# Kernel optimization log

Hardware: AMD Instinct MI355X
Metric: run time of the kernel (lower is better)

Reference implementation:

```python
import math
import jax, jax.numpy as jnp
import numpy as np

B, S, HID = 2, 2048, 1024
NH, HD = 16, 64            # num heads, head dim (HID = NH*HD)
NB, MAXD = 32, 128         # relative attention buckets / max distance
Q_SCALING = 1.0


def setup_inputs() -> dict:
    key = jax.random.key(0)
    ks = jax.random.split(key, 6)
    return {
        "hidden_states": jax.random.normal(ks[0], (B, S, HID), dtype=jnp.float32),
        "w_qkv": jax.random.normal(ks[1], (HID, 3 * HID), dtype=jnp.float32) * 0.02,
        "b_qkv": jax.random.normal(ks[2], (3 * HID,), dtype=jnp.float32) * 0.02,
        "w_dense": jax.random.normal(ks[3], (HID, HID), dtype=jnp.float32) * 0.02,
        "b_dense": jax.random.normal(ks[4], (HID,), dtype=jnp.float32) * 0.02,
        "rel_attn_table": jax.random.normal(ks[5], (NH, NB), dtype=jnp.float32) * 0.02,
    }


def _relative_position_bucket(q_len, k_len, num_buckets, max_distance):
    # Bidirectional T5-style buckets, matching compute_relative_bias.
    ctx = jnp.arange(q_len, dtype=jnp.int32)[:, None]
    mem = jnp.arange(k_len, dtype=jnp.int32)[None, :]
    rel = mem - ctx                                     # [Q, K]
    nb = num_buckets // 2
    buckets = jnp.where(rel > 0, nb, 0)
    rel = jnp.abs(rel)
    max_exact = nb // 2
    is_small = rel < max_exact
    # log path (clamp to >=1 to avoid log(0); masked by is_small anyway)
    tmp = jnp.log(jnp.maximum(rel, 1).astype(jnp.float32) / max_exact)
    large = tmp / math.log(max_distance / max_exact) * (nb - max_exact)
    large = max_exact + large.astype(jnp.int32)
    large = jnp.minimum(large, nb - 1)
    return buckets + jnp.where(is_small, rel, large)    # [Q, K]


def reference(hidden_states, w_qkv, b_qkv, w_dense, b_dense, rel_attn_table):
    b, s, _ = hidden_states.shape
    qkv = hidden_states @ w_qkv + b_qkv                 # [B, S, 3*HID]
    q, k, v = jnp.split(qkv, 3, axis=-1)
    q = q.reshape(b, s, NH, HD)
    k = k.reshape(b, s, NH, HD)
    v = v.reshape(b, s, NH, HD)

    norm = Q_SCALING * math.sqrt(HD)
    scores = jnp.einsum("bqhd,bkhd->bhqk", q, k) / norm  # [B, H, S, S]

    buckets = _relative_position_bucket(s, s, NB, MAXD)  # [Q, K] int32
    bias = rel_attn_table[:, buckets]                    # [H, Q, K]
    scores = scores + bias[None]

    probs = jax.nn.softmax(scores, axis=-1)
    ctx = jnp.einsum("bhqk,bkhd->bqhd", probs, v).reshape(b, s, HID)
    return ctx @ w_dense + b_dense
```

## Files before the change

### kernel.cpp

```cpp
#include <hip/hip_runtime.h>
#include <hip/hip_bf16.h>
#include <math.h>

#define S_ 2048

typedef __attribute__((ext_vector_type(8))) short bf16x8;
typedef __attribute__((ext_vector_type(4))) float f32x4;
typedef __attribute__((ext_vector_type(8))) unsigned short u16x8;
typedef __attribute__((ext_vector_type(4))) unsigned short u16x4;

__device__ inline unsigned short f2bf(float f) {
  union { float f; unsigned u; } x; x.f = f;
  unsigned r = x.u + 0x7fff + ((x.u >> 16) & 1);
  return (unsigned short)(r >> 16);
}

__device__ __forceinline__ float exp2_raw(float x) {
  float r;
  asm("v_exp_f32 %0, %1" : "=v"(r) : "v"(x));
  return r;
}

__device__ __forceinline__ void gll16(const unsigned short* g, unsigned short* l) {
  __builtin_amdgcn_global_load_lds(
      (const __attribute__((address_space(1))) unsigned int*)g,
      (__attribute__((address_space(3))) unsigned int*)l, 16, 0, 0);
}

__global__ void bias_table_kernel(const float* __restrict__ table,
                                  float* __restrict__ biasTab) {
  int idx = blockIdx.x * blockDim.x + threadIdx.x;
  if (idx >= 16 * 4096) return;
  int h = idx >> 12;
  int r = idx & 4095;
  int rel = r - 2047;
  int bucket = rel > 0 ? 16 : 0;
  int ar = rel < 0 ? -rel : rel;
  if (ar < 8) {
    bucket += ar;
  } else {
    float tmp = logf((float)ar / 8.0f);
    float lf = tmp / 2.7725887222397811f * 8.0f;
    int large = 8 + (int)lf;
    bucket += (large < 15 ? large : 15);
  }
  biasTab[idx] = table[h * 32 + bucket] * 1.44269504088896f;
}

__global__ __launch_bounds__(256) void cvt_bf16_kernel(
    const float* __restrict__ in, unsigned short* __restrict__ out, int n8) {
  int i = blockIdx.x * blockDim.x + threadIdx.x;
  if (i >= n8) return;
  float4 a = ((const float4*)in)[i * 2];
  float4 b = ((const float4*)in)[i * 2 + 1];
  u16x8 o;
  o[0] = f2bf(a.x); o[1] = f2bf(a.y); o[2] = f2bf(a.z); o[3] = f2bf(a.w);
  o[4] = f2bf(b.x); o[5] = f2bf(b.y); o[6] = f2bf(b.z); o[7] = f2bf(b.w);
  *(u16x8*)&out[(size_t)i * 8] = o;
}

__global__ __launch_bounds__(256) void transpose_cvt_kernel(
    const float* __restrict__ in, unsigned short* __restrict__ out,
    int K, int N) {
  __shared__ unsigned short tile[64][72];
  const int k0 = blockIdx.y * 64, n0 = blockIdx.x * 64;
  const int tid = threadIdx.x;
  const int rr = tid >> 4, cc = (tid & 15) * 4;
#pragma unroll
  for (int p = 0; p < 4; ++p) {
    int k = rr + p * 16;
    float4 v = *(const float4*)&in[(size_t)(k0 + k) * N + n0 + cc];
    tile[k][cc + 0] = f2bf(v.x);
    tile[k][cc + 1] = f2bf(v.y);
    tile[k][cc + 2] = f2bf(v.z);
    tile[k][cc + 3] = f2bf(v.w);
  }
  __syncthreads();
#pragma unroll
  for (int p = 0; p < 4; ++p) {
    int n = rr + p * 16;
    u16x4 o;
    o[0] = tile[cc + 0][n];
    o[1] = tile[cc + 1][n];
    o[2] = tile[cc + 2][n];
    o[3] = tile[cc + 3][n];
    *(u16x4*)&out[(size_t)(n0 + n) * K + k0 + cc] = o;
  }
}

template <bool BF16OUT>
__global__ __launch_bounds__(256) void gemm_mfma_kernel(
    const unsigned short* __restrict__ A, const unsigned short* __restrict__ Bt,
    const float* __restrict__ bias, void* __restrict__ Cout,
    int M, int N, int K) {
  __shared__ __align__(16) unsigned short As[128 * 32];
  __shared__ __align__(16) unsigned short Bs[128 * 32];
  const int tid = threadIdx.x;
  const int wave = tid >> 6, lane = tid & 63;
  const int lg = lane >> 4, lr = lane & 15;
  const int m0 = blockIdx.y * 128, n0 = blockIdx.x * 128;
  const int wm = (wave & 1) * 64, wn = (wave >> 1) * 64;

  f32x4 acc[4][4] = {};

  const int r0 = tid >> 2;
  const int sw = ((tid & 3) ^ (r0 & 3)) << 3;
  const unsigned short* aP0 = A + (size_t)(m0 + r0) * K + sw;
  const unsigned short* aP1 = A + (size_t)(m0 + 64 + r0) * K + sw;
  const unsigned short* bP0 = Bt + (size_t)(n0 + r0) * K + sw;
  const unsigned short* bP1 = Bt + (size_t)(n0 + 64 + r0) * K + sw;
  unsigned short* ldsA0 = &As[(tid & ~63) * 8];
  unsigned short* ldsA1 = &As[(256 + (tid & ~63)) * 8];
  unsigned short* ldsB0 = &Bs[(tid & ~63) * 8];
  unsigned short* ldsB1 = &Bs[(256 + (tid & ~63)) * 8];

  const int swz = (lg ^ (lr & 3)) << 3;

  for (int kt = 0; kt < K; kt += 32) {
    __syncthreads();
    gll16(aP0 + kt, ldsA0);
    gll16(aP1 + kt, ldsA1);
    gll16(bP0 + kt, ldsB0);
    gll16(bP1 + kt, ldsB1);
    __syncthreads();
    bf16x8 af[4], bfr[4];
#pragma unroll
    for (int t = 0; t < 4; ++t) {
      af[t]  = *(const bf16x8*)&As[(wm + t * 16 + lr) * 32 + swz];
      bfr[t] = *(const bf16x8*)&Bs[(wn + t * 16 + lr) * 32 + swz];
    }
#pragma unroll
    for (int i = 0; i < 4; ++i)
#pragma unroll
      for (int j = 0; j < 4; ++j)
        acc[i][j] = __builtin_amdgcn_mfma_f32_16x16x32_bf16(
            af[i], bfr[j], acc[i][j], 0, 0, 0);
  }

  float bv[4];
#pragma unroll
  for (int j = 0; j < 4; ++j) bv[j] = bias[n0 + wn + j * 16 + lr];
#pragma unroll
  for (int i = 0; i < 4; ++i) {
#pragma unroll
    for (int j = 0; j < 4; ++j) {
#pragma unroll
      for (int r = 0; r < 4; ++r) {
        int row = m0 + wm + i * 16 + lg * 4 + r;
        int col = n0 + wn + j * 16 + lr;
        float val = acc[i][j][r] + bv[j];
        if constexpr (BF16OUT)
          ((unsigned short*)Cout)[(size_t)row * N + col] = f2bf(val);
        else
          ((float*)Cout)[(size_t)row * N + col] = val;
      }
    }
  }
}

__global__ __launch_bounds__(256) void vperm_kernel(
    const unsigned short* __restrict__ qkvb, unsigned short* __restrict__ vP) {
  const int t = blockIdx.x, h = blockIdx.y, bb = blockIdx.z;
  __shared__ unsigned short tile[64][72];
  const int tid = threadIdx.x;
  {
    int k = tid >> 2, c = (tid & 3) * 16;
    const unsigned short* src =
        qkvb + (size_t)(bb * S_ + t * 64 + k) * 3072 + 2048 + h * 64 + c;
    *(bf16x8*)&tile[k][c] = *(const bf16x8*)src;
    *(bf16x8*)&tile[k][c + 8] = *(const bf16x8*)(src + 8);
  }
  __syncthreads();
  const int d = tid >> 2, m0 = (tid & 3) * 16;
  unsigned short* dst =
      vP + ((size_t)((bb * 16 + h) * 64 + d)) * S_ + t * 64 + m0;
#pragma unroll
  for (int half = 0; half < 2; ++half) {
    u16x8 o;
#pragma unroll
    for (int j = 0; j < 8; ++j) {
      int m = m0 + half * 8 + j;
      int phys_s = m >> 3, e = m & 7;
      int s = phys_s ^ (d & 7);
      int w = s >> 2, lg = s & 3;
      int kw = w * 32 + (e >> 2) * 16 + lg * 4 + (e & 3);
      o[j] = tile[kw][d];
    }
    *(u16x8*)(dst + half * 8) = o;
  }
}

__global__ __launch_bounds__(512) void attn_mfma6_kernel(
    const unsigned short* __restrict__ qkvb, const unsigned short* __restrict__ vP,
    const float* __restrict__ biasTab, unsigned short* __restrict__ ctxb) {
  const int wg0 = blockIdx.x;
  const int wg = (wg0 & 7) * 64 + (wg0 >> 3);
  const int qt = wg & 15;
  const int h  = (wg >> 4) & 15;
  const int bb = wg >> 8;

  const int tid = threadIdx.x;
  const int wave = tid >> 6;
  const int lane = tid & 63;
  const int lg = lane >> 4;
  const int lr = lane & 15;

  __shared__ __align__(16) unsigned short Klds[2][4096];
  __shared__ __align__(16) unsigned short Vlds[2][4096];
  __shared__ float biasW[2][192];

  const int q0 = qt * 128;
  const int qw = q0 + wave * 16;
  const float SCL = 0.125f * 1.44269504088896f;
  const float THR = 11.5415603f;

  bf16x8 qf[2];
#pragma unroll
  for (int kh = 0; kh < 2; ++kh)
    qf[kh] = *(const bf16x8*)(qkvb +
        (size_t)(bb * S_ + qw + lr) * 3072 + h * 64 + kh * 32 + lg * 8);

  float mrun = -1e30f;
  float lpart = 0.f;
  f32x4 ov[4] = {};

  const int kk = tid >> 3, kpb = tid & 7;
  const unsigned short* kptr = qkvb + (size_t)(bb * S_ + kk) * 3072 + 1024 +
                               h * 64 + (kpb ^ (kk & 7)) * 8;
  const unsigned short* vptr = vP + ((size_t)((bb * 16 + h) * 64 + (tid >> 3))) * S_ +
                               (tid & 7) * 8;
  const float* btabH = biasTab + h * 4096 + 2047;

  auto nonuni = [&](int tt) {
    int rl = tt * 64 - q0;
    return !((rl - 127 >= 91) || (rl + 63 <= -91));
  };

  gll16(kptr, &Klds[0][(tid & ~63) * 8]);
  gll16(vptr, &Vlds[0][(tid & ~63) * 8]);
  if (nonuni(0) && tid < 192) biasW[0][tid] = btabH[-q0 - 127 + tid];

  for (int t = 0; t < 32; ++t) {
    const int cur = t & 1;
    __syncthreads();

    if (t < 31) {
      const size_t kadv = (size_t)(t + 1) * 64 * 3072;
      gll16(kptr + kadv, &Klds[cur ^ 1][(tid & ~63) * 8]);
      gll16(vptr + (t + 1) * 64, &Vlds[cur ^ 1][(tid & ~63) * 8]);
      if (nonuni(t + 1) && tid < 192)
        biasW[cur ^ 1][tid] = btabH[(t + 1) * 64 - q0 - 127 + tid];
    }

    f32x4 sc[4] = {};
#pragma unroll
    for (int kt = 0; kt < 4; ++kt) {
      const unsigned short* kr = &Klds[cur][(kt * 16 + lr) * 64];
      bf16x8 kf0 = *(const bf16x8*)(kr + ((lg)     ^ (lr & 7)) * 8);
      bf16x8 kf1 = *(const bf16x8*)(kr + ((4 + lg) ^ (lr & 7)) * 8);
      sc[kt] = __builtin_amdgcn_mfma_f32_16x16x32_bf16(kf0, qf[0], sc[kt], 0, 0, 0);
      sc[kt] = __builtin_amdgcn_mfma_f32_16x16x32_bf16(kf1, qf[1], sc[kt], 0, 0, 0);
    }

    float pp[4][4];
    if (nonuni(t)) {
      const int bidx = 127 + lg * 4 - wave * 16 - lr;
#pragma unroll
      for (int kt = 0; kt < 4; ++kt)
#pragma unroll
        for (int r = 0; r < 4; ++r)
          pp[kt][r] = sc[kt][r] * SCL + biasW[cur][bidx + kt * 16 + r];
    } else {
      const float cb = btabH[t * 64 - q0];
#pragma unroll
      for (int kt = 0; kt < 4; ++kt)
#pragma unroll
        for (int r = 0; r < 4; ++r)
          pp[kt][r] = sc[kt][r] * SCL + cb;
    }

    float mx[8];
#pragma unroll
    for (int i = 0; i < 8; ++i)
      mx[i] = fmaxf(pp[i >> 1][(i & 1) * 2], pp[i >> 1][(i & 1) * 2 + 1]);
    float m01 = fmaxf(mx[0], mx[1]), m23 = fmaxf(mx[2], mx[3]);
    float m45 = fmaxf(mx[4], mx[5]), m67 = fmaxf(mx[6], mx[7]);
    float tm = fmaxf(fmaxf(m01, m23), fmaxf(m45, m67));

    if (!__all(tm <= mrun + THR)) {
      tm = fmaxf(tm, __shfl_xor(tm, 16));
      tm = fmaxf(tm, __shfl_xor(tm, 32));
      float mn = fmaxf(mrun, tm);
      float sfv = exp2_raw(mrun - mn);
      mrun = mn;
      lpart *= sfv;
#pragma unroll
      for (int r = 0; r < 4; ++r) {
        float sq = __shfl(sfv, (lane & 48) | (lg * 4 + r));
#pragma unroll
        for (int db = 0; db < 4; ++db) ov[db][r] *= sq;
      }
    }

#pragma unroll
    for (int kt = 0; kt < 4; ++kt)
#pragma unroll
      for (int r = 0; r < 4; ++r)
        pp[kt][r] = exp2_raw(pp[kt][r] - mrun);
    float s8[8];
#pragma unroll
    for (int i = 0; i < 8; ++i)
      s8[i] = pp[i >> 1][(i & 1) * 2] + pp[i >> 1][(i & 1) * 2 + 1];
    float s01 = s8[0] + s8[1], s23 = s8[2] + s8[3];
    float s45 = s8[4] + s8[5], s67 = s8[6] + s8[7];
    lpart += (s01 + s23) + (s45 + s67);

    union { bf16x8 v; unsigned u[4]; } pk[2];
#pragma unroll
    for (int kh = 0; kh < 2; ++kh) {
      asm("v_cvt_pk_bf16_f32 %0, %1, %2"
          : "=v"(pk[kh].u[0]) : "v"(pp[2 * kh][0]), "v"(pp[2 * kh][1]));
      asm("v_cvt_pk_bf16_f32 %0, %1, %2"
          : "=v"(pk[kh].u[1]) : "v"(pp[2 * kh][2]), "v"(pp[2 * kh][3]));
      asm("v_cvt_pk_bf16_f32 %0, %1, %2"
          : "=v"(pk[kh].u[2]) : "v"(pp[2 * kh + 1][0]), "v"(pp[2 * kh + 1][1]));
      asm("v_cvt_pk_bf16_f32 %0, %1, %2"
          : "=v"(pk[kh].u[3]) : "v"(pp[2 * kh + 1][2]), "v"(pp[2 * kh + 1][3]));
    }

#pragma unroll
    for (int kh = 0; kh < 2; ++kh)
#pragma unroll
      for (int db = 0; db < 4; ++db) {
        bf16x8 vf = *(const bf16x8*)&Vlds[cur][
            (db * 16 + lr) * 64 + ((4 * kh + lg) ^ (lr & 7)) * 8];
        ov[db] = __builtin_amdgcn_mfma_f32_16x16x32_bf16(
            pk[kh].v, vf, ov[db], 0, 0, 0);
      }
  }

  float lsum = lpart;
  lsum += __shfl_xor(lsum, 16);
  lsum += __shfl_xor(lsum, 32);
  float invl = 1.0f / lsum;
#pragma unroll
  for (int r = 0; r < 4; ++r) {
    float iv = __shfl(invl, (lane & 48) | (lg * 4 + r));
    size_t row = (size_t)(bb * S_ + qw + lg * 4 + r);
#pragma unroll
    for (int db = 0; db < 4; ++db)
      ctxb[row * 1024 + h * 64 + db * 16 + lr] = f2bf(ov[db][r] * iv);
  }
}

extern "C" void kernel_launch(void* const* d_in, const int* in_sizes, int n_in,
                              void* d_out, int out_size, void* d_ws, size_t ws_size,
                              hipStream_t stream) {
  const float* hs      = (const float*)d_in[0];
  const float* w_qkv   = (const float*)d_in[1];
  const float* b_qkv   = (const float*)d_in[2];
  const float* w_dense = (const float*)d_in[3];
  const float* b_dense = (const float*)d_in[4];
  const float* rtab    = (const float*)d_in[5];
  float* out = (float*)d_out;

  char* ws = (char*)d_ws;
  unsigned short* qkvb = (unsigned short*)ws;
  unsigned short* ctxb = (unsigned short*)(ws + (((size_t)24) << 20));
  unsigned short* hsb  = (unsigned short*)(ws + (((size_t)32) << 20));
  unsigned short* wqT  = (unsigned short*)(ws + (((size_t)40) << 20));
  unsigned short* wdT  = (unsigned short*)(ws + (((size_t)46) << 20));
  unsigned short* vP   = (unsigned short*)(ws + (((size_t)48) << 20));
  float* biasTab       = (float*)(ws + (((size_t)56) << 20));

  hipLaunchKernelGGL(bias_table_kernel, dim3(256), dim3(256), 0, stream,
                     rtab, biasTab);
  hipLaunchKernelGGL(cvt_bf16_kernel, dim3(2048), dim3(256), 0, stream,
                     hs, hsb, 4096 * 1024 / 8);
  hipLaunchKernelGGL(transpose_cvt_kernel, dim3(48, 16), dim3(256), 0, stream,
                     w_qkv, wqT, 1024, 3072);
  hipLaunchKernelGGL(transpose_cvt_kernel, dim3(16, 16), dim3(256), 0, stream,
                     w_dense, wdT, 1024, 1024);
  hipLaunchKernelGGL((gemm_mfma_kernel<true>), dim3(24, 32), dim3(256), 0, stream,
                     hsb, wqT, b_qkv, (void*)qkvb, 4096, 3072, 1024);
  hipLaunchKernelGGL(vperm_kernel, dim3(32, 16, 2), dim3(256), 0, stream,
                     qkvb, vP);
  hipLaunchKernelGGL(attn_mfma6_kernel, dim3(512), dim3(512), 0, stream,
                     qkvb, vP, biasTab, ctxb);
  hipLaunchKernelGGL((gemm_mfma_kernel<false>), dim3(8, 32), dim3(256), 0, stream,
                     ctxb, wdT, b_dense, (void*)out, 4096, 1024, 1024);
}
```

Before: 146.8 us.

## Fuse prologue kernels, swizzle GEMM block order, raise MFMA wave priority

Merges the bias-table, hidden-state conversion and two weight-transpose kernels into one prologue launch that dispatches by block index, removing three launches and the idle gaps between them. The GEMM remaps flat block IDs so that consecutive blocks are spread across eight groups, with the aim of better L2/XCD locality. It also wraps the MFMA sections in the GEMM and attention loops with s_setprio so waves issuing matrix ops get scheduling priority. The prologue mixes branches with different shared-memory needs in one kernel, and the swizzle assumes the block count divides by 8.

Result: faster. 136.0 us (-7.3%).

```diff
diff --git a/kernel.cpp b/kernel.cpp
--- a/kernel.cpp
+++ b/kernel.cpp
@@ -27,44 +27,10 @@
       (__attribute__((address_space(3))) unsigned int*)l, 16, 0, 0);
 }
 
-__global__ void bias_table_kernel(const float* __restrict__ table,
-                                  float* __restrict__ biasTab) {
-  int idx = blockIdx.x * blockDim.x + threadIdx.x;
-  if (idx >= 16 * 4096) return;
-  int h = idx >> 12;
-  int r = idx & 4095;
-  int rel = r - 2047;
-  int bucket = rel > 0 ? 16 : 0;
-  int ar = rel < 0 ? -rel : rel;
-  if (ar < 8) {
-    bucket += ar;
-  } else {
-    float tmp = logf((float)ar / 8.0f);
-    float lf = tmp / 2.7725887222397811f * 8.0f;
-    int large = 8 + (int)lf;
-    bucket += (large < 15 ? large : 15);
-  }
-  biasTab[idx] = table[h * 32 + bucket] * 1.44269504088896f;
-}
-
-__global__ __launch_bounds__(256) void cvt_bf16_kernel(
-    const float* __restrict__ in, unsigned short* __restrict__ out, int n8) {
-  int i = blockIdx.x * blockDim.x + threadIdx.x;
-  if (i >= n8) return;
-  float4 a = ((const float4*)in)[i * 2];
-  float4 b = ((const float4*)in)[i * 2 + 1];
-  u16x8 o;
-  o[0] = f2bf(a.x); o[1] = f2bf(a.y); o[2] = f2bf(a.z); o[3] = f2bf(a.w);
-  o[4] = f2bf(b.x); o[5] = f2bf(b.y); o[6] = f2bf(b.z); o[7] = f2bf(b.w);
-  *(u16x8*)&out[(size_t)i * 8] = o;
-}
-
-__global__ __launch_bounds__(256) void transpose_cvt_kernel(
+__device__ __forceinline__ void transpose_tile(
     const float* __restrict__ in, unsigned short* __restrict__ out,
-    int K, int N) {
-  __shared__ unsigned short tile[64][72];
-  const int k0 = blockIdx.y * 64, n0 = blockIdx.x * 64;
-  const int tid = threadIdx.x;
+    int K, int N, int bx, int by, int tid, unsigned short (*tile)[72]) {
+  const int k0 = by * 64, n0 = bx * 64;
   const int rr = tid >> 4, cc = (tid & 15) * 4;
 #pragma unroll
   for (int p = 0; p < 4; ++p) {
@@ -85,6 +51,47 @@
     o[2] = tile[cc + 2][n];
     o[3] = tile[cc + 3][n];
     *(u16x4*)&out[(size_t)(n0 + n) * K + k0 + cc] = o;
+  }
+}
+
+__global__ __launch_bounds__(256) void prologue_kernel(
+    const float* __restrict__ hs, unsigned short* __restrict__ hsb,
+    const float* __restrict__ w_qkv, unsigned short* __restrict__ wqT,
+    const float* __restrict__ w_dense, unsigned short* __restrict__ wdT,
+    const float* __restrict__ table, float* __restrict__ biasTab) {
+  __shared__ unsigned short tile[64][72];
+  const int blk = blockIdx.x;
+  const int tid = threadIdx.x;
+  if (blk < 2048) {
+    int i = blk * 256 + tid;
+    float4 a = ((const float4*)hs)[i * 2];
+    float4 b = ((const float4*)hs)[i * 2 + 1];
+    u16x8 o;
+    o[0] = f2bf(a.x); o[1] = f2bf(a.y); o[2] = f2bf(a.z); o[3] = f2bf(a.w);
+    o[4] = f2bf(b.x); o[5] = f2bf(b.y); o[6] = f2bf(b.z); o[7] = f2bf(b.w);
+    *(u16x8*)&hsb[(size_t)i * 8] = o;
+  } else if (blk < 2816) {
+    int t = blk - 2048;
+    transpose_tile(w_qkv, wqT, 1024, 3072, t % 48, t / 48, tid, tile);
+  } else if (blk < 3072) {
+    int t = blk - 2816;
+    transpose_tile(w_dense, wdT, 1024, 1024, t % 16, t / 16, tid, tile);
+  } else {
+    int idx = (blk - 3072) * 256 + tid;
+    int h = idx >> 12;
+    int r = idx & 4095;
+    int rel = r - 2047;
+    int bucket = rel > 0 ? 16 : 0;
+    int ar = rel < 0 ? -rel : rel;
+    if (ar < 8) {
+      bucket += ar;
+    } else {
+      float tmp = logf((float)ar / 8.0f);
+      float lf = tmp / 2.7725887222397811f * 8.0f;
+      int large = 8 + (int)lf;
+      bucket += (large < 15 ? large : 15);
+    }
+    biasTab[idx] = table[h * 32 + bucket] * 1.44269504088896f;
   }
 }
 
@@ -98,7 +105,11 @@
   const int tid = threadIdx.x;
   const int wave = tid >> 6, lane = tid & 63;
   const int lg = lane >> 4, lr = lane & 15;
-  const int m0 = blockIdx.y * 128, n0 = blockIdx.x * 128;
+  const int nbx = gridDim.x;
+  const int flat = blockIdx.y * nbx + blockIdx.x;
+  const int cpx = (nbx * gridDim.y) >> 3;
+  const int swzid = (flat & 7) * cpx + (flat >> 3);
+  const int m0 = (swzid / nbx) * 128, n0 = (swzid % nbx) * 128;
   const int wm = (wave & 1) * 64, wn = (wave >> 1) * 64;
 
   f32x4 acc[4][4] = {};
@@ -129,12 +140,14 @@
       af[t]  = *(const bf16x8*)&As[(wm + t * 16 + lr) * 32 + swz];
       bfr[t] = *(const bf16x8*)&Bs[(wn + t * 16 + lr) * 32 + swz];
     }
+    __builtin_amdgcn_s_setprio(1);
 #pragma unroll
     for (int i = 0; i < 4; ++i)
 #pragma unroll
       for (int j = 0; j < 4; ++j)
         acc[i][j] = __builtin_amdgcn_mfma_f32_16x16x32_bf16(
             af[i], bfr[j], acc[i][j], 0, 0, 0);
+    __builtin_amdgcn_s_setprio(0);
   }
 
   float bv[4];
@@ -253,6 +266,7 @@
     }
 
     f32x4 sc[4] = {};
+    __builtin_amdgcn_s_setprio(1);
 #pragma unroll
     for (int kt = 0; kt < 4; ++kt) {
       const unsigned short* kr = &Klds[cur][(kt * 16 + lr) * 64];
@@ -261,6 +275,7 @@
       sc[kt] = __builtin_amdgcn_mfma_f32_16x16x32_bf16(kf0, qf[0], sc[kt], 0, 0, 0);
       sc[kt] = __builtin_amdgcn_mfma_f32_16x16x32_bf16(kf1, qf[1], sc[kt], 0, 0, 0);
     }
+    __builtin_amdgcn_s_setprio(0);
 
     float pp[4][4];
     if (nonuni(t)) {
@@ -328,6 +343,7 @@
           : "=v"(pk[kh].u[3]) : "v"(pp[2 * kh + 1][2]), "v"(pp[2 * kh + 1][3]));
     }
 
+    __builtin_amdgcn_s_setprio(1);
 #pragma unroll
     for (int kh = 0; kh < 2; ++kh)
 #pragma unroll
@@ -337,6 +353,7 @@
         ov[db] = __builtin_amdgcn_mfma_f32_16x16x32_bf16(
             pk[kh].v, vf, ov[db], 0, 0, 0);
       }
+    __builtin_amdgcn_s_setprio(0);
   }
 
   float lsum = lpart;
@@ -373,14 +390,8 @@
   unsigned short* vP   = (unsigned short*)(ws + (((size_t)48) << 20));
   float* biasTab       = (float*)(ws + (((size_t)56) << 20));
 
-  hipLaunchKernelGGL(bias_table_kernel, dim3(256), dim3(256), 0, stream,
-                     rtab, biasTab);
-  hipLaunchKernelGGL(cvt_bf16_kernel, dim3(2048), dim3(256), 0, stream,
-                     hs, hsb, 4096 * 1024 / 8);
-  hipLaunchKernelGGL(transpose_cvt_kernel, dim3(48, 16), dim3(256), 0, stream,
-                     w_qkv, wqT, 1024, 3072);
-  hipLaunchKernelGGL(transpose_cvt_kernel, dim3(16, 16), dim3(256), 0, stream,
-                     w_dense, wdT, 1024, 1024);
+  hipLaunchKernelGGL(prologue_kernel, dim3(3328), dim3(256), 0, stream,
+                     hs, hsb, w_qkv, wqT, w_dense, wdT, rtab, biasTab);
   hipLaunchKernelGGL((gemm_mfma_kernel<true>), dim3(24, 32), dim3(256), 0, stream,
                      hsb, wqT, b_qkv, (void*)qkvb, 4096, 3072, 1024);
   hipLaunchKernelGGL(vperm_kernel, dim3(32, 16, 2), dim3(256), 0, stream,
```
